# Optimization experiments

Hardware: AMD Instinct MI355X
Metric: run time of the kernel (lower is better)

Reference implementation:

```python
import jax, jax.numpy as jnp
import numpy as np

H = 8            # head_size (hard-coded in the original forward)
BB = 0.6         # balance_bias
NEG = -1e9


def masked_softmax(x, m, axis=-1):
    # softmax over `axis`, zero out masked entries, renormalize
    p = jax.nn.softmax(x, axis=axis)
    p = p * m
    return p / (p.sum(axis=axis, keepdims=True) + 1e-13)


def setup_inputs():
    key = jax.random.key(0)
    ks = jax.random.split(key, 12)
    B, B0, V, A, Hd = 8, 2, 384, 384, 512
    S = V + A
    s = 1.0 / np.sqrt(Hd)
    return {
        'q': jax.random.normal(ks[0], (B, S, Hd), jnp.float32),
        'k': jax.random.normal(ks[1], (B, S, Hd), jnp.float32),
        'v': jax.random.normal(ks[2], (B, S, Hd), jnp.float32),
        'mask': jnp.ones((B, S, 1), jnp.float32),
        'depth_value': jax.random.uniform(ks[3], (B0, V), jnp.float32),
        'coord_3d': jax.random.normal(ks[4], (B, V, 3), jnp.float32),
        'va_v_mask': jnp.ones((B, V, 1), jnp.float32),
        'va_a_mask': jnp.ones((B, A, 1), jnp.float32),
        'mean_depth_value': jax.random.uniform(ks[5], (B, A), jnp.float32),
        'Wq': jax.random.normal(ks[6], (Hd, Hd), jnp.float32) * s,
        'bq': jnp.zeros((Hd,), jnp.float32),
        'Wk': jax.random.normal(ks[7], (Hd, Hd), jnp.float32) * s,
        'bk': jnp.zeros((Hd,), jnp.float32),
        'Wv': jax.random.normal(ks[8], (Hd, Hd), jnp.float32) * s,
        'bv': jnp.zeros((Hd,), jnp.float32),
        'Wo': jax.random.normal(ks[9], (Hd, Hd), jnp.float32) * s,
        'bo': jnp.zeros((Hd,), jnp.float32),
    }


def reference(q, k, v, mask, depth_value, coord_3d, va_v_mask, va_a_mask,
              mean_depth_value, Wq, bq, Wk, bk, Wv, bv, Wo, bo):
    B, S, Hd = q.shape
    d = Hd // H
    scale = d ** (-0.5)
    V = va_v_mask.shape[1]
    A = va_a_mask.shape[1]
    B0 = depth_value.shape[0]
    rep = B // B0  # = 4 in the original code

    qh = (q @ Wq + bq).reshape(B, S, H, d).transpose(0, 2, 1, 3)  # [B,H,S,d]
    kh = (k @ Wk + bk).reshape(B, S, H, d).transpose(0, 2, 1, 3)
    vh = (v @ Wv + bv).reshape(B, S, H, d).transpose(0, 2, 1, 3)

    m = mask[:, None]                      # [B,1,S,1]
    mask4 = m * jnp.swapaxes(m, 2, 3)      # [B,1,S,S] (broadcasts over heads)

    x = jnp.einsum('bhqd,bhkd->bhqk', qh, kh) * scale  # [B,H,S,S]

    # visual-visual depth bias
    dv = depth_value[:, :, None]                       # [B0,V,1]
    diff = jnp.abs(dv - jnp.swapaxes(dv, 1, 2))        # [B0,V,V]
    diff = jnp.repeat(diff, rep, axis=0)[:, None]      # [B,1,V,V]
    self_mask = 1.0 - jnp.eye(V, dtype=x.dtype)
    depth_term = jnp.abs(x[:, :, :V, :V]) * (jnp.exp(-diff) - BB) * self_mask  # [B,H,V,V]

    # audio->visual attention map (pre-bias scores)
    x_av = x[:, :, V:, :V]                             # [B,H,A,V]
    m_av = mask4[:, :, V:, :V]
    att_score_av = jnp.where(m_av > 0, x_av, NEG)
    att_map_av = masked_softmax(att_score_av, m_av, axis=3)

    # audio-visual depth bias (mean_depth_value branch)
    tdv = jnp.repeat(jnp.swapaxes(dv, 1, 2), rep, axis=0)           # [B,1,V]
    diff_va = jnp.abs(mean_depth_value[:, :, None] - tdv)[:, None]  # [B,1,A,V]
    depth_av_term = jnp.abs(x_av) * (jnp.exp(-diff_va) - BB)        # [B,H,A,V]

    # assemble bias matrix: [:V,:V]=depth_term, [V:,:V]=depth_av_term, rest 0
    top = jnp.concatenate([depth_term, jnp.zeros((B, H, V, S - V), x.dtype)], axis=3)
    bot = jnp.concatenate([depth_av_term, jnp.zeros((B, H, A, S - V), x.dtype)], axis=3)
    bias = jnp.concatenate([top, bot], axis=2)         # [B,H,S,S]

    x = x + bias
    att_score = jnp.where(mask4 > 0, x, NEG)
    att_map = masked_softmax(att_score, mask4 * jnp.ones((1, H, 1, 1), x.dtype), axis=3)
    out = jnp.einsum('bhqk,bhkd->bhqd', att_map, vh)   # [B,H,S,d]

    # auxiliary depth mean via the a->v attention map
    dv_rep = jnp.repeat(depth_value, rep, axis=0)      # [B,V]
    md = jnp.einsum('bhav,bv->bha', att_map_av, dv_rep)
    md = md.mean(axis=1)                               # [B,A]
    md = md.sum(axis=-1) / va_a_mask[:, :, 0].sum(axis=-1)  # [B]
    md = jnp.broadcast_to(md[:, None], (B, A))

    out = out.transpose(0, 2, 1, 3).reshape(B, S, H * d)
    out = out @ Wo + bo
    return out, att_score, att_map, md
```

## Files before the change

kernel.cpp:

```cpp
#include <hip/hip_runtime.h>
#include <hip/hip_bf16.h>
#include <cstdint>
#include <cstddef>

namespace {
constexpr int B  = 8;
constexpr int S  = 768;
constexpr int V  = 384;
constexpr int A  = 384;
constexpr int H  = 8;
constexpr int D  = 64;
constexpr int HD = 512;
constexpr float SCALE = 0.125f;
constexpr float BBC   = 0.6f;
constexpr float NEGV  = -1000000000.0f;
constexpr size_t N_QH = (size_t)B * H * S * D;
}

using short8 = __attribute__((ext_vector_type(8))) short;
using f32x4  = __attribute__((ext_vector_type(4))) float;

static __device__ __forceinline__ unsigned short f2bf(float f) {
  union { float f; unsigned int u; } v; v.f = f;
  unsigned int r = v.u + 0x7FFFu + ((v.u >> 16) & 1u);
  return (unsigned short)(r >> 16);
}
static __device__ __forceinline__ f32x4 mfma16(short8 a, short8 b, f32x4 c) {
  return __builtin_amdgcn_mfma_f32_16x16x32_bf16(a, b, c, 0, 0, 0);
}

__global__ __launch_bounds__(256) void prep_all(
    const float* __restrict__ Wq, const float* __restrict__ Wk,
    const float* __restrict__ Wv, const float* __restrict__ Wo,
    const float* __restrict__ q, const float* __restrict__ k,
    const float* __restrict__ v,
    unsigned short* __restrict__ wt, unsigned short* __restrict__ xs)
{
  const int id = blockIdx.x;
  const int t = threadIdx.x;
  if (id < 256) {
    __shared__ float tile[64][68];
    const int z = id >> 6, tl = id & 63;
    const int k0 = (tl >> 3) * 64, n0 = (tl & 7) * 64;
    const float* W = (z == 0) ? Wq : (z == 1) ? Wk : (z == 2) ? Wv : Wo;
    unsigned short* WTh = wt + (size_t)z * 524288;
    unsigned short* WTl = WTh + 262144;
#pragma unroll
    for (int u = 0; u < 4; ++u) {
      int idx = u * 256 + t;
      int r = idx >> 4, c4 = (idx & 15) * 4;
      *(float4*)&tile[r][c4] = *(const float4*)&W[(size_t)(k0 + r) * 512 + n0 + c4];
    }
    __syncthreads();
#pragma unroll
    for (int u = 0; u < 4; ++u) {
      int idx = u * 256 + t;
      int n = idx >> 4, kq = (idx & 15) * 4;
      unsigned int uh[4], ul[4];
#pragma unroll
      for (int j = 0; j < 4; ++j) {
        float x = tile[kq + j][n];
        unsigned int ux = __float_as_uint(x);
        uh[j] = ux >> 16;
        float r = x - __uint_as_float(ux & 0xFFFF0000u);
        ul[j] = __float_as_uint(r) >> 16;
      }
      *(uint2*)&WTh[(size_t)(n0 + n) * 512 + k0 + kq] =
          make_uint2(uh[0] | (uh[1] << 16), uh[2] | (uh[3] << 16));
      *(uint2*)&WTl[(size_t)(n0 + n) * 512 + k0 + kq] =
          make_uint2(ul[0] | (ul[1] << 16), ul[2] | (ul[3] << 16));
    }
  } else {
    const int m = id - 256;
    const int z = m / 96, rb = m % 96;
    const float* X = (z == 0) ? q : (z == 1) ? k : v;
    unsigned short* xh = xs + (size_t)z * N_QH;
#pragma unroll 4
    for (int u = 0; u < 32; ++u) {
      int idx = u * 256 + t;
      int row = idx >> 7, c = (idx & 127) * 4;
      size_t base = (size_t)(rb * 64 + row) * 512 + c;
      float4 xv = *(const float4*)&X[base];
      unsigned int h0 = f2bf(xv.x), h1 = f2bf(xv.y), h2 = f2bf(xv.z), h3 = f2bf(xv.w);
      *(uint2*)&xh[base] = make_uint2(h0 | (h1 << 16), h2 | (h3 << 16));
    }
  }
}

__global__ __launch_bounds__(256) void qkv_mfma(
    const unsigned short* __restrict__ xs, const unsigned short* __restrict__ wt,
    const float* __restrict__ bq, const float* __restrict__ bk,
    const float* __restrict__ bv,
    unsigned short* __restrict__ qh, unsigned short* __restrict__ kh,
    unsigned short* __restrict__ vhT)
{
  __shared__ unsigned short Ah[64][40];
  __shared__ unsigned short Bh[64][40];
  __shared__ unsigned short Bl[64][40];
  const int lin = ((blockIdx.x & 7) * 288) + (blockIdx.x >> 3);
  const int n0 = (lin & 7) * 64;
  const int gidx = lin >> 3;
  const int mt = gidx % 96, z = gidx / 96;
  const int m0 = mt * 64;
  const unsigned short* Xh = xs + (size_t)z * N_QH;
  const unsigned short* WTh = wt + (size_t)z * 524288;
  const unsigned short* WTl = WTh + 262144;
  const float* bias = (z == 0) ? bq : (z == 1) ? bk : bv;
  const int t = threadIdx.x, w = t >> 6, lane = t & 63;
  const int l15 = lane & 15, g = lane >> 4;
  const int bb = m0 / S;
  f32x4 acc[4] = {};

  const int srow = t >> 2, skq = (t & 3) * 8;
  for (int k0 = 0; k0 < 512; k0 += 32) {
    __syncthreads();
    *(short8*)&Ah[srow][skq] = *(const short8*)&Xh[(size_t)(m0 + srow) * 512 + k0 + skq];
    *(short8*)&Bh[srow][skq] = *(const short8*)&WTh[(size_t)(n0 + srow) * 512 + k0 + skq];
    *(short8*)&Bl[srow][skq] = *(const short8*)&WTl[(size_t)(n0 + srow) * 512 + k0 + skq];
    __syncthreads();
    if (z != 2) {
      short8 ah = *(short8*)&Ah[w * 16 + l15][g * 8];
#pragma unroll
      for (int tn = 0; tn < 4; ++tn) {
        short8 bh_ = *(short8*)&Bh[tn * 16 + l15][g * 8];
        short8 bl_ = *(short8*)&Bl[tn * 16 + l15][g * 8];
        acc[tn] = mfma16(ah, bl_, acc[tn]);
        acc[tn] = mfma16(ah, bh_, acc[tn]);
      }
    } else {
      short8 wh = *(short8*)&Bh[w * 16 + l15][g * 8];
      short8 wl = *(short8*)&Bl[w * 16 + l15][g * 8];
#pragma unroll
      for (int tm = 0; tm < 4; ++tm) {
        short8 xf = *(short8*)&Ah[tm * 16 + l15][g * 8];
        acc[tm] = mfma16(wl, xf, acc[tm]);
        acc[tm] = mfma16(wh, xf, acc[tm]);
      }
    }
  }

  if (z != 2) {
    unsigned short* Y = (z == 0) ? qh : kh;
#pragma unroll
    for (int tn = 0; tn < 4; ++tn) {
      const int c = n0 + tn * 16 + l15;
      const float bi = bias[c];
      const int h = c >> 6, d = c & 63;
#pragma unroll
      for (int r = 0; r < 4; ++r) {
        const int mm = m0 + w * 16 + g * 4 + r;
        const int s = mm - bb * S;
        Y[((size_t)(bb * H + h) * S + s) * D + d] = f2bf(acc[tn][r] + bi);
      }
    }
  } else {
#pragma unroll
    for (int tm = 0; tm < 4; ++tm) {
      const int mcol = m0 + tm * 16 + l15;
      const int s = mcol - bb * S;
#pragma unroll
      for (int r = 0; r < 4; ++r) {
        const int n = n0 + w * 16 + g * 4 + r;
        const int h = n >> 6, d = n & 63;
        vhT[((size_t)(bb * H + h) * D + d) * S + s] = f2bf(acc[tm][r] + bias[n]);
      }
    }
  }
}

__global__ __launch_bounds__(256, 4) void fused_attn(
    const unsigned short* __restrict__ qh, const unsigned short* __restrict__ kh,
    const unsigned short* __restrict__ vhT,
    const float* __restrict__ mask, const float* __restrict__ depth_value,
    const float* __restrict__ mean_depth,
    float* __restrict__ att_score, float* __restrict__ att_map,
    unsigned short* __restrict__ ctx, float* __restrict__ md_rows)
{
  __shared__ unsigned short Ps[16][768];
  __shared__ float mcol[768];
  __shared__ float dvcol[384];
  __shared__ float pmax[16][4];
  __shared__ float psum[16][4];
  __shared__ float psem[16][4];
  __shared__ float asmd[16][2];
  __shared__ float mxA[16], rdA[16], drefsA[16], mrwA[16];

  const int id = blockIdx.x;
  const int rest = id >> 3;
  const int rt = rest % 48;
  const int bh = (id & 7) + 8 * (rest / 48);
  const int b = bh >> 3, b0 = b >> 2;
  const int r0 = rt * 16;
  const int t = threadIdx.x;
  const int w = t >> 6;
  const int lane = t & 63;
  const int l15 = lane & 15, g = lane >> 4;
  const bool avblk = (r0 >= V);

  for (int j = t; j < 768; j += 256) mcol[j] = mask[(size_t)b * S + j];
  for (int j = t; j < 384; j += 256) dvcol[j] = depth_value[(size_t)b0 * V + j];
  if (t < 16) {
    const int row = r0 + t;
    drefsA[t] = (row < V) ? depth_value[(size_t)b0 * V + row]
                          : mean_depth[(size_t)b * A + (row - V)];
    mrwA[t] = mask[(size_t)b * S + row];
  }

  short8 qf[2];
#pragma unroll
  for (int ks = 0; ks < 2; ++ks)
    qf[ks] = *(const short8*)&qh[((size_t)bh * S + r0 + l15) * D + ks * 32 + g * 8];

  f32x4 acc[12] = {};
#pragma unroll
  for (int tn = 0; tn < 12; ++tn) {
    const int col = w * 192 + tn * 16 + l15;
#pragma unroll
    for (int ks = 0; ks < 2; ++ks) {
      short8 kf = *(const short8*)&kh[((size_t)bh * S + col) * D + ks * 32 + g * 8];
      acc[tn] = mfma16(qf[ks], kf, acc[tn]);
    }
  }
  __syncthreads();

  const bool biasw = (w < 2);
  float mcr[12], dvc[12];
#pragma unroll
  for (int tn = 0; tn < 12; ++tn) {
    const int col = w * 192 + tn * 16 + l15;
    mcr[tn] = mcol[col];
    dvc[tn] = biasw ? dvcol[col] : 0.f;
  }

#pragma unroll
  for (int r = 0; r < 4; ++r) {
    const int lrow = g * 4 + r;
    const int row = r0 + lrow;
    const float mr = mrwA[lrow];
    const float dref = drefsA[lrow];
    float* srow = &att_score[((size_t)bh * S + row) * S];
#pragma unroll
    for (int tn = 0; tn < 12; ++tn) {
      const int col = w * 192 + tn * 16 + l15;
      float x = acc[tn][r] * SCALE;
      if (biasw) {
        float gg = __expf(-fabsf(dref - dvc[tn])) - BBC;
        float bb2 = fabsf(x) * gg;
        if (row == col) bb2 = 0.f;
        x += bb2;
      }
      x = (mr * mcr[tn] > 0.f) ? x : NEGV;
      srow[col] = x;
      acc[tn][r] = x;
    }
  }

#pragma unroll
  for (int r = 0; r < 4; ++r) {
    float v = NEGV;
#pragma unroll
    for (int tn = 0; tn < 12; ++tn) v = fmaxf(v, acc[tn][r]);
#pragma unroll
    for (int o = 1; o < 16; o <<= 1) v = fmaxf(v, __shfl_xor(v, o, 16));
    if (l15 == 0) pmax[g * 4 + r][w] = v;
  }
  __syncthreads();
  if (t < 16)
    mxA[t] = fmaxf(fmaxf(pmax[t][0], pmax[t][1]), fmaxf(pmax[t][2], pmax[t][3]));
  __syncthreads();

  if (avblk) {
    if (biasw) {
#pragma unroll
      for (int r = 0; r < 4; ++r) {
        const int lrow = g * 4 + r;
        const float mdv = drefsA[lrow];
        const float mr = mrwA[lrow];
        const float amx = fmaxf(2.5f * mxA[lrow], 0.f);
        float se = 0.f, sem = 0.f, smd = 0.f;
#pragma unroll
        for (int tn = 0; tn < 12; ++tn) {
          float post = acc[tn][r];
          float gg = __expf(-fabsf(mdv - dvc[tn])) - BBC;
          float pre = post / (post > 0.f ? 1.f + gg : 1.f - gg);
          float pm = mr * mcr[tn];
          pre = (pm > 0.f) ? pre : NEGV;
          float e = __expf(pre - amx);
          se += e; sem += e * pm; smd += e * pm * dvc[tn];
        }
#pragma unroll
        for (int o = 1; o < 16; o <<= 1) {
          se += __shfl_xor(se, o, 16);
          sem += __shfl_xor(sem, o, 16);
          smd += __shfl_xor(smd, o, 16);
        }
        if (l15 == 0) { psum[lrow][w] = se; psem[lrow][w] = sem; asmd[lrow][w] = smd; }
      }
    }
    __syncthreads();
    if (t < 16) {
      float se = psum[t][0] + psum[t][1];
      float sem = psem[t][0] + psem[t][1];
      float smd = asmd[t][0] + asmd[t][1];
      md_rows[(size_t)bh * A + (r0 + t - V)] = smd / (sem + 1e-13f * se);
    }
    __syncthreads();
  }

#pragma unroll
  for (int r = 0; r < 4; ++r) {
    const int lrow = g * 4 + r;
    const float mx = mxA[lrow];
    const float mr = mrwA[lrow];
    float se = 0.f, sem = 0.f;
#pragma unroll
    for (int tn = 0; tn < 12; ++tn) {
      float e = __expf(acc[tn][r] - mx);
      acc[tn][r] = e;
      se += e; sem += e * (mr * mcr[tn]);
    }
#pragma unroll
    for (int o = 1; o < 16; o <<= 1) {
      se += __shfl_xor(se, o, 16);
      sem += __shfl_xor(sem, o, 16);
    }
    if (l15 == 0) { psum[lrow][w] = se; psem[lrow][w] = sem; }
  }
  __syncthreads();
  if (t < 16) {
    float se = psum[t][0] + psum[t][1] + psum[t][2] + psum[t][3];
    float sem = psem[t][0] + psem[t][1] + psem[t][2] + psem[t][3];
    rdA[t] = 1.f / (sem + 1e-13f * se);
  }
  __syncthreads();

#pragma unroll
  for (int r = 0; r < 4; ++r) {
    const int lrow = g * 4 + r;
    const int row = r0 + lrow;
    const float rden = rdA[lrow];
    const float mr = mrwA[lrow];
    float* prow = &att_map[((size_t)bh * S + row) * S];
    const int swz = (lrow & 7) << 4;
#pragma unroll
    for (int tn = 0; tn < 12; ++tn) {
      const int col = w * 192 + tn * 16 + l15;
      float p = acc[tn][r] * (mr * mcr[tn]) * rden;
      prow[col] = p;
      Ps[lrow][col ^ swz] = f2bf(p);
    }
  }
  __syncthreads();

  {
    const int aswz = (l15 & 7) << 4;
    f32x4 pacc = {};
    const unsigned short* vcol = &vhT[((size_t)bh * D + w * 16 + l15) * S];
#pragma unroll 8
    for (int kk = 0; kk < 24; ++kk) {
      short8 a = *(short8*)&Ps[l15][(kk * 32 + g * 8) ^ aswz];
      short8 bv = *(const short8*)&vcol[kk * 32 + g * 8];
      pacc = mfma16(a, bv, pacc);
    }
#pragma unroll
    for (int r = 0; r < 4; ++r) {
      const int row = r0 + g * 4 + r;
      ctx[((size_t)bh * S + row) * D + w * 16 + l15] = f2bf(pacc[r]);
    }
  }
}

__global__ __launch_bounds__(256) void gemm_out(
    const unsigned short* __restrict__ Xb, const unsigned short* __restrict__ WTh,
    const unsigned short* __restrict__ WTl, const float* __restrict__ bias,
    float* __restrict__ Yf,
    const float* __restrict__ md_rows, const float* __restrict__ va_a_mask,
    float* __restrict__ md_out)
{
  const int t = threadIdx.x;
  if (blockIdx.x >= 768) {
    __shared__ float red0[256];
    __shared__ float red1[256];
    const int b = blockIdx.x - 768;
    float s1 = 0.f, s2 = 0.f;
    for (int u = t; u < H * A; u += 256) s1 += md_rows[(size_t)b * H * A + u];
    for (int u = t; u < A; u += 256) s2 += va_a_mask[(size_t)b * A + u];
    red0[t] = s1; red1[t] = s2;
    __syncthreads();
    for (int o = 128; o > 0; o >>= 1) {
      if (t < o) { red0[t] += red0[t + o]; red1[t] += red1[t + o]; }
      __syncthreads();
    }
    const float val = red0[0] / ((float)H * red1[0]);
    for (int u = t; u < A; u += 256) md_out[(size_t)b * A + u] = val;
    return;
  }
  __shared__ unsigned short Ah[64][40];
  __shared__ unsigned short Bh[64][40];
  __shared__ unsigned short Bl[64][40];
  const int lin = ((blockIdx.x & 7) * 96) + (blockIdx.x >> 3);
  const int n0 = (lin & 7) * 64;
  const int m0 = (lin >> 3) * 64;
  const int w = t >> 6, lane = t & 63;
  const int l15 = lane & 15, g = lane >> 4;
  const int bb = m0 / S;
  f32x4 acc[4] = {};
  const int srow = t >> 2, skq = (t & 3) * 8;
  for (int k0 = 0; k0 < 512; k0 += 32) {
    __syncthreads();
    {
      const int s = m0 + srow - bb * S;
      const int h = k0 >> 6, d = (k0 & 63) + skq;
      *(short8*)&Ah[srow][skq] = *(const short8*)&Xb[((size_t)(bb * H + h) * S + s) * D + d];
    }
    *(short8*)&Bh[srow][skq] = *(const short8*)&WTh[(size_t)(n0 + srow) * 512 + k0 + skq];
    *(short8*)&Bl[srow][skq] = *(const short8*)&WTl[(size_t)(n0 + srow) * 512 + k0 + skq];
    __syncthreads();
    short8 ah = *(short8*)&Ah[w * 16 + l15][g * 8];
#pragma unroll
    for (int tn = 0; tn < 4; ++tn) {
      short8 bh_ = *(short8*)&Bh[tn * 16 + l15][g * 8];
      short8 bl_ = *(short8*)&Bl[tn * 16 + l15][g * 8];
      acc[tn] = mfma16(ah, bl_, acc[tn]);
      acc[tn] = mfma16(ah, bh_, acc[tn]);
    }
  }
#pragma unroll
  for (int tn = 0; tn < 4; ++tn) {
    const int c = n0 + tn * 16 + l15;
    const float bi = bias[c];
#pragma unroll
    for (int r = 0; r < 4; ++r) {
      const int m = m0 + w * 16 + g * 4 + r;
      Yf[(size_t)m * 512 + c] = acc[tn][r] + bi;
    }
  }
}

extern "C" void kernel_launch(void* const* d_in, const int* in_sizes, int n_in,
                              void* d_out, int out_size, void* d_ws, size_t ws_size,
                              hipStream_t stream) {
  const float* q           = (const float*)d_in[0];
  const float* k           = (const float*)d_in[1];
  const float* v           = (const float*)d_in[2];
  const float* mask        = (const float*)d_in[3];
  const float* depth_value = (const float*)d_in[4];
  const float* va_a_mask   = (const float*)d_in[7];
  const float* mean_depth  = (const float*)d_in[8];
  const float* Wq = (const float*)d_in[9];
  const float* bq = (const float*)d_in[10];
  const float* Wk = (const float*)d_in[11];
  const float* bk = (const float*)d_in[12];
  const float* Wv = (const float*)d_in[13];
  const float* bv = (const float*)d_in[14];
  const float* Wo = (const float*)d_in[15];
  const float* bo = (const float*)d_in[16];

  unsigned short* wsu = (unsigned short*)d_ws;
  unsigned short* qh  = wsu;
  unsigned short* kh  = wsu + N_QH;
  unsigned short* vhT = wsu + 2 * N_QH;
  unsigned short* ctx = qh;
  unsigned short* wt  = wsu + 3 * N_QH;
  float* md_rows = (float*)(wsu + 3 * N_QH + 4 * 524288);

  float* out       = (float*)d_out;
  float* att_score = out + (size_t)B * S * HD;
  float* att_map   = att_score + (size_t)B * H * S * S;
  float* md_out    = att_map + (size_t)B * H * S * S;

  unsigned short* xs = (unsigned short*)att_score;

  prep_all<<<544, 256, 0, stream>>>(Wq, Wk, Wv, Wo, q, k, v, wt, xs);
  qkv_mfma<<<2304, 256, 0, stream>>>(xs, wt, bq, bk, bv, qh, kh, vhT);
  fused_attn<<<3072, 256, 0, stream>>>(qh, kh, vhT, mask, depth_value, mean_depth,
                                       att_score, att_map, ctx, md_rows);
  gemm_out<<<776, 256, 0, stream>>>(ctx, wt + 3 * 524288, wt + 3 * 524288 + 262144,
                                    bo, out, md_rows, va_a_mask, md_out);
}
```

Before: 184.1 us.

## Drop split-bf16 weight correction, convert inputs in GEMM, use nontemporal stores

Removes the hi/lo bf16 weight split so the QKV and output projections issue one MFMA per tile instead of two. The separate q/k/v to bf16 conversion pass is dropped, and the QKV GEMM now reads fp32 inputs and converts them in registers or LDS. The output GEMM reads the A operand directly from global memory instead of staging it through LDS. The large att_score and att_map writes use nontemporal stores to reduce cache pollution. The cost is lower precision in the projections, since the weights are now plain bf16 without the residual term, which may hurt accuracy against the fp32 reference.

```diff
diff --git a/kernel.cpp b/kernel.cpp
--- a/kernel.cpp
+++ b/kernel.cpp
@@ -28,83 +28,62 @@
 static __device__ __forceinline__ f32x4 mfma16(short8 a, short8 b, f32x4 c) {
   return __builtin_amdgcn_mfma_f32_16x16x32_bf16(a, b, c, 0, 0, 0);
 }
-
-__global__ __launch_bounds__(256) void prep_all(
+static __device__ __forceinline__ short8 pack_bf8(float4 a, float4 b) {
+  union { short8 s; uint4 u; } r;
+  r.u.x = (unsigned)f2bf(a.x) | ((unsigned)f2bf(a.y) << 16);
+  r.u.y = (unsigned)f2bf(a.z) | ((unsigned)f2bf(a.w) << 16);
+  r.u.z = (unsigned)f2bf(b.x) | ((unsigned)f2bf(b.y) << 16);
+  r.u.w = (unsigned)f2bf(b.z) | ((unsigned)f2bf(b.w) << 16);
+  return r.s;
+}
+
+__global__ __launch_bounds__(256) void prep_w(
     const float* __restrict__ Wq, const float* __restrict__ Wk,
     const float* __restrict__ Wv, const float* __restrict__ Wo,
+    unsigned short* __restrict__ wt)
+{
+  __shared__ float tile[64][68];
+  const int id = blockIdx.x;
+  const int z = id >> 6, tl = id & 63;
+  const int k0 = (tl >> 3) * 64, n0 = (tl & 7) * 64;
+  const float* W = (z == 0) ? Wq : (z == 1) ? Wk : (z == 2) ? Wv : Wo;
+  unsigned short* WT = wt + (size_t)z * 262144;
+  const int t = threadIdx.x;
+#pragma unroll
+  for (int u = 0; u < 4; ++u) {
+    int idx = u * 256 + t;
+    int r = idx >> 4, c4 = (idx & 15) * 4;
+    *(float4*)&tile[r][c4] = *(const float4*)&W[(size_t)(k0 + r) * 512 + n0 + c4];
+  }
+  __syncthreads();
+#pragma unroll
+  for (int u = 0; u < 4; ++u) {
+    int idx = u * 256 + t;
+    int n = idx >> 4, kq = (idx & 15) * 4;
+    unsigned int h0 = f2bf(tile[kq + 0][n]), h1 = f2bf(tile[kq + 1][n]);
+    unsigned int h2 = f2bf(tile[kq + 2][n]), h3 = f2bf(tile[kq + 3][n]);
+    *(uint2*)&WT[(size_t)(n0 + n) * 512 + k0 + kq] =
+        make_uint2(h0 | (h1 << 16), h2 | (h3 << 16));
+  }
+}
+
+__global__ __launch_bounds__(256) void qkv_mfma(
     const float* __restrict__ q, const float* __restrict__ k,
-    const float* __restrict__ v,
-    unsigned short* __restrict__ wt, unsigned short* __restrict__ xs)
-{
-  const int id = blockIdx.x;
-  const int t = threadIdx.x;
-  if (id < 256) {
-    __shared__ float tile[64][68];
-    const int z = id >> 6, tl = id & 63;
-    const int k0 = (tl >> 3) * 64, n0 = (tl & 7) * 64;
-    const float* W = (z == 0) ? Wq : (z == 1) ? Wk : (z == 2) ? Wv : Wo;
-    unsigned short* WTh = wt + (size_t)z * 524288;
-    unsigned short* WTl = WTh + 262144;
-#pragma unroll
-    for (int u = 0; u < 4; ++u) {
-      int idx = u * 256 + t;
-      int r = idx >> 4, c4 = (idx & 15) * 4;
-      *(float4*)&tile[r][c4] = *(const float4*)&W[(size_t)(k0 + r) * 512 + n0 + c4];
-    }
-    __syncthreads();
-#pragma unroll
-    for (int u = 0; u < 4; ++u) {
-      int idx = u * 256 + t;
-      int n = idx >> 4, kq = (idx & 15) * 4;
-      unsigned int uh[4], ul[4];
-#pragma unroll
-      for (int j = 0; j < 4; ++j) {
-        float x = tile[kq + j][n];
-        unsigned int ux = __float_as_uint(x);
-        uh[j] = ux >> 16;
-        float r = x - __uint_as_float(ux & 0xFFFF0000u);
-        ul[j] = __float_as_uint(r) >> 16;
-      }
-      *(uint2*)&WTh[(size_t)(n0 + n) * 512 + k0 + kq] =
-          make_uint2(uh[0] | (uh[1] << 16), uh[2] | (uh[3] << 16));
-      *(uint2*)&WTl[(size_t)(n0 + n) * 512 + k0 + kq] =
-          make_uint2(ul[0] | (ul[1] << 16), ul[2] | (ul[3] << 16));
-    }
-  } else {
-    const int m = id - 256;
-    const int z = m / 96, rb = m % 96;
-    const float* X = (z == 0) ? q : (z == 1) ? k : v;
-    unsigned short* xh = xs + (size_t)z * N_QH;
-#pragma unroll 4
-    for (int u = 0; u < 32; ++u) {
-      int idx = u * 256 + t;
-      int row = idx >> 7, c = (idx & 127) * 4;
-      size_t base = (size_t)(rb * 64 + row) * 512 + c;
-      float4 xv = *(const float4*)&X[base];
-      unsigned int h0 = f2bf(xv.x), h1 = f2bf(xv.y), h2 = f2bf(xv.z), h3 = f2bf(xv.w);
-      *(uint2*)&xh[base] = make_uint2(h0 | (h1 << 16), h2 | (h3 << 16));
-    }
-  }
-}
-
-__global__ __launch_bounds__(256) void qkv_mfma(
-    const unsigned short* __restrict__ xs, const unsigned short* __restrict__ wt,
+    const float* __restrict__ v, const unsigned short* __restrict__ wt,
     const float* __restrict__ bq, const float* __restrict__ bk,
     const float* __restrict__ bv,
     unsigned short* __restrict__ qh, unsigned short* __restrict__ kh,
     unsigned short* __restrict__ vhT)
 {
-  __shared__ unsigned short Ah[64][40];
   __shared__ unsigned short Bh[64][40];
-  __shared__ unsigned short Bl[64][40];
+  __shared__ unsigned short Ax[64][40];
   const int lin = ((blockIdx.x & 7) * 288) + (blockIdx.x >> 3);
   const int n0 = (lin & 7) * 64;
   const int gidx = lin >> 3;
   const int mt = gidx % 96, z = gidx / 96;
   const int m0 = mt * 64;
-  const unsigned short* Xh = xs + (size_t)z * N_QH;
-  const unsigned short* WTh = wt + (size_t)z * 524288;
-  const unsigned short* WTl = WTh + 262144;
+  const float* X = (z == 0) ? q : (z == 1) ? k : v;
+  const unsigned short* WT = wt + (size_t)z * 262144;
   const float* bias = (z == 0) ? bq : (z == 1) ? bk : bv;
   const int t = threadIdx.x, w = t >> 6, lane = t & 63;
   const int l15 = lane & 15, g = lane >> 4;
@@ -114,26 +93,28 @@
   const int srow = t >> 2, skq = (t & 3) * 8;
   for (int k0 = 0; k0 < 512; k0 += 32) {
     __syncthreads();
-    *(short8*)&Ah[srow][skq] = *(const short8*)&Xh[(size_t)(m0 + srow) * 512 + k0 + skq];
-    *(short8*)&Bh[srow][skq] = *(const short8*)&WTh[(size_t)(n0 + srow) * 512 + k0 + skq];
-    *(short8*)&Bl[srow][skq] = *(const short8*)&WTl[(size_t)(n0 + srow) * 512 + k0 + skq];
+    *(short8*)&Bh[srow][skq] = *(const short8*)&WT[(size_t)(n0 + srow) * 512 + k0 + skq];
+    if (z == 2) {
+      float4 x0 = *(const float4*)&X[(size_t)(m0 + srow) * 512 + k0 + skq];
+      float4 x1 = *(const float4*)&X[(size_t)(m0 + srow) * 512 + k0 + skq + 4];
+      *(short8*)&Ax[srow][skq] = pack_bf8(x0, x1);
+    }
     __syncthreads();
     if (z != 2) {
-      short8 ah = *(short8*)&Ah[w * 16 + l15][g * 8];
+      const size_t abase = (size_t)(m0 + w * 16 + l15) * 512 + k0 + g * 8;
+      float4 a0 = *(const float4*)&X[abase];
+      float4 a1 = *(const float4*)&X[abase + 4];
+      short8 ah = pack_bf8(a0, a1);
 #pragma unroll
       for (int tn = 0; tn < 4; ++tn) {
         short8 bh_ = *(short8*)&Bh[tn * 16 + l15][g * 8];
-        short8 bl_ = *(short8*)&Bl[tn * 16 + l15][g * 8];
-        acc[tn] = mfma16(ah, bl_, acc[tn]);
         acc[tn] = mfma16(ah, bh_, acc[tn]);
       }
     } else {
       short8 wh = *(short8*)&Bh[w * 16 + l15][g * 8];
-      short8 wl = *(short8*)&Bl[w * 16 + l15][g * 8];
 #pragma unroll
       for (int tm = 0; tm < 4; ++tm) {
-        short8 xf = *(short8*)&Ah[tm * 16 + l15][g * 8];
-        acc[tm] = mfma16(wl, xf, acc[tm]);
+        short8 xf = *(short8*)&Ax[tm * 16 + l15][g * 8];
         acc[tm] = mfma16(wh, xf, acc[tm]);
       }
     }
@@ -250,7 +231,7 @@
         x += bb2;
       }
       x = (mr * mcr[tn] > 0.f) ? x : NEGV;
-      srow[col] = x;
+      __builtin_nontemporal_store(x, &srow[col]);
       acc[tn][r] = x;
     }
   }
@@ -346,7 +327,7 @@
     for (int tn = 0; tn < 12; ++tn) {
       const int col = w * 192 + tn * 16 + l15;
       float p = acc[tn][r] * (mr * mcr[tn]) * rden;
-      prow[col] = p;
+      __builtin_nontemporal_store(p, &prow[col]);
       Ps[lrow][col ^ swz] = f2bf(p);
     }
   }
@@ -371,9 +352,8 @@
 }
 
 __global__ __launch_bounds__(256) void gemm_out(
-    const unsigned short* __restrict__ Xb, const unsigned short* __restrict__ WTh,
-    const unsigned short* __restrict__ WTl, const float* __restrict__ bias,
-    float* __restrict__ Yf,
+    const unsigned short* __restrict__ Xb, const unsigned short* __restrict__ WT,
+    const float* __restrict__ bias, float* __restrict__ Yf,
     const float* __restrict__ md_rows, const float* __restrict__ va_a_mask,
     float* __restrict__ md_out)
 {
@@ -395,9 +375,7 @@
     for (int u = t; u < A; u += 256) md_out[(size_t)b * A + u] = val;
     return;
   }
-  __shared__ unsigned short Ah[64][40];
   __shared__ unsigned short Bh[64][40];
-  __shared__ unsigned short Bl[64][40];
   const int lin = ((blockIdx.x & 7) * 96) + (blockIdx.x >> 3);
   const int n0 = (lin & 7) * 64;
   const int m0 = (lin >> 3) * 64;
@@ -408,20 +386,14 @@
   const int srow = t >> 2, skq = (t & 3) * 8;
   for (int k0 = 0; k0 < 512; k0 += 32) {
     __syncthreads();
-    {
-      const int s = m0 + srow - bb * S;
-      const int h = k0 >> 6, d = (k0 & 63) + skq;
-      *(short8*)&Ah[srow][skq] = *(const short8*)&Xb[((size_t)(bb * H + h) * S + s) * D + d];
-    }
-    *(short8*)&Bh[srow][skq] = *(const short8*)&WTh[(size_t)(n0 + srow) * 512 + k0 + skq];
-    *(short8*)&Bl[srow][skq] = *(const short8*)&WTl[(size_t)(n0 + srow) * 512 + k0 + skq];
-    __syncthreads();
-    short8 ah = *(short8*)&Ah[w * 16 + l15][g * 8];
+    *(short8*)&Bh[srow][skq] = *(const short8*)&WT[(size_t)(n0 + srow) * 512 + k0 + skq];
+    __syncthreads();
+    const int s = m0 + w * 16 + l15 - bb * S;
+    const int h = k0 >> 6, d = (k0 & 63) + g * 8;
+    short8 ah = *(const short8*)&Xb[((size_t)(bb * H + h) * S + s) * D + d];
 #pragma unroll
     for (int tn = 0; tn < 4; ++tn) {
       short8 bh_ = *(short8*)&Bh[tn * 16 + l15][g * 8];
-      short8 bl_ = *(short8*)&Bl[tn * 16 + l15][g * 8];
-      acc[tn] = mfma16(ah, bl_, acc[tn]);
       acc[tn] = mfma16(ah, bh_, acc[tn]);
     }
   }
@@ -462,19 +434,17 @@
   unsigned short* vhT = wsu + 2 * N_QH;
   unsigned short* ctx = qh;
   unsigned short* wt  = wsu + 3 * N_QH;
-  float* md_rows = (float*)(wsu + 3 * N_QH + 4 * 524288);
+  float* md_rows = (float*)(wsu + 3 * N_QH + 4 * 262144);
 
   float* out       = (float*)d_out;
   float* att_score = out + (size_t)B * S * HD;
   float* att_map   = att_score + (size_t)B * H * S * S;
   float* md_out    = att_map + (size_t)B * H * S * S;
 
-  unsigned short* xs = (unsigned short*)att_score;
-
-  prep_all<<<544, 256, 0, stream>>>(Wq, Wk, Wv, Wo, q, k, v, wt, xs);
-  qkv_mfma<<<2304, 256, 0, stream>>>(xs, wt, bq, bk, bv, qh, kh, vhT);
+  prep_w<<<256, 256, 0, stream>>>(Wq, Wk, Wv, Wo, wt);
+  qkv_mfma<<<2304, 256, 0, stream>>>(q, k, v, wt, bq, bk, bv, qh, kh, vhT);
   fused_attn<<<3072, 256, 0, stream>>>(qh, kh, vhT, mask, depth_value, mean_depth,
                                        att_score, att_map, ctx, md_rows);
-  gemm_out<<<776, 256, 0, stream>>>(ctx, wt + 3 * 524288, wt + 3 * 524288 + 262144,
-                                    bo, out, md_rows, va_a_mask, md_out);
-}
+  gemm_out<<<776, 256, 0, stream>>>(ctx, wt + 3 * 262144, bo, out,
+                                    md_rows, va_a_mask, md_out);
+}
```

New measurement: 172.2 us. -6.5%, faster.
